# Performance work log

Measured on AMD Instinct MI355X. Metric: run time of the kernel, lower is better.

The kernel has to match this reference:

```python
import jax, jax.numpy as jnp
import numpy as np

N_NODES = 100000

def _gcn_norm(edge_index, num_nodes):
    # PyG GCNConv: add self-loops, symmetric normalization deg^-1/2 A_hat deg^-1/2
    loop = jnp.arange(num_nodes, dtype=edge_index.dtype)
    src = jnp.concatenate([edge_index[0], loop])  # [E+N]
    dst = jnp.concatenate([edge_index[1], loop])  # [E+N]
    deg = jax.ops.segment_sum(jnp.ones(dst.shape[0], jnp.float32), dst, num_segments=num_nodes)
    dis = jnp.where(deg > 0, jax.lax.rsqrt(deg), 0.0)
    norm = dis[src] * dis[dst]  # [E+N]
    return src, dst, norm

def _gcn_layer(x, W, b, src, dst, norm, num_nodes):
    xw = x @ W                                   # [N, H] dense GEMM first (out_dim <= in_dim)
    msg = xw[src] * norm[:, None]                # gather + scale per edge
    out = jax.ops.segment_sum(msg, dst, num_segments=num_nodes)  # scatter-add
    return out + b

def setup_inputs() -> dict:
    key = jax.random.key(0)
    ks = jax.random.split(key, 6)
    E = 1600000
    return {
        "x": jax.random.normal(ks[0], (N_NODES, 512), jnp.float32),
        "edge_index": jax.random.randint(ks[1], (2, E), 0, N_NODES, dtype=jnp.int64),
        "W1": jax.random.normal(ks[2], (512, 256), jnp.float32) * 0.04,
        "b1": jnp.zeros((256,), jnp.float32),
        "W2": jax.random.normal(ks[3], (256, 256), jnp.float32) * 0.06,
        "b2": jnp.zeros((256,), jnp.float32),
        "fc_w": jax.random.normal(ks[4], (256, 128), jnp.float32) * 0.06,
        "fc_b": jnp.zeros((128,), jnp.float32),
    }

def reference(x, edge_index, W1, b1, W2, b2, fc_w, fc_b):
    src, dst, norm = _gcn_norm(edge_index, N_NODES)
    h = jax.nn.relu(_gcn_layer(x, W1, b1, src, dst, norm, N_NODES))
    h = jax.nn.relu(_gcn_layer(h, W2, b2, src, dst, norm, N_NODES))
    return h @ fc_w + fc_b
```

## Files before the change

kernel.cpp:

```cpp
#include <hip/hip_runtime.h>


#define N_NODES 100000
constexpr int D_IN  = 512;
constexpr int D_H   = 256;
constexpr int D_OUT = 128;

typedef _Float16 f16x8 __attribute__((ext_vector_type(8)));
typedef _Float16 f16x4 __attribute__((ext_vector_type(4)));
typedef float f32x4 __attribute__((ext_vector_type(4)));


__global__ __launch_bounds__(256) void deg_count_k(const int* __restrict__ dst,
                                                   int* __restrict__ deg,
                                                   int* __restrict__ pe, int E) {
  int i = (blockIdx.x * 256 + threadIdx.x) * 4;
  if (i + 3 < E) {
    int4 d = *(const int4*)(dst + i);
    int4 p;
    p.x = atomicAdd(&deg[d.x], 1);
    p.y = atomicAdd(&deg[d.y], 1);
    p.z = atomicAdd(&deg[d.z], 1);
    p.w = atomicAdd(&deg[d.w], 1);
    *(int4*)(pe + i) = p;
  } else {
    for (int t = i; t < E; ++t) pe[t] = atomicAdd(&deg[dst[t]], 1);
  }
}

__global__ __launch_bounds__(256) void scan1_k(const int* __restrict__ deg,
                                               int* __restrict__ off,
                                               int* __restrict__ bsum,
                                               float* __restrict__ dis, int n) {
  __shared__ int ts[256];
  const int tid = threadIdx.x;
  const int base = blockIdx.x * 1024 + tid * 4;
  int v[4];
#pragma unroll
  for (int t = 0; t < 4; ++t) v[t] = (base + t < n) ? deg[base + t] : 0;
#pragma unroll
  for (int t = 0; t < 4; ++t)
    if (base + t < n) dis[base + t] = rsqrtf((float)v[t] + 1.0f);
  const int tot = v[0] + v[1] + v[2] + v[3];
  ts[tid] = tot;
  __syncthreads();
  for (int o = 1; o < 256; o <<= 1) {
    int t = (tid >= o) ? ts[tid - o] : 0;
    __syncthreads();
    ts[tid] += t;
    __syncthreads();
  }
  int run = ts[tid] - tot;
#pragma unroll
  for (int t = 0; t < 4; ++t) {
    if (base + t < n) off[base + t] = run;
    run += v[t];
  }
  if (tid == 255) bsum[blockIdx.x] = ts[255];
}

__global__ __launch_bounds__(128) void scan2_k(int* __restrict__ bsum, int nb) {
  __shared__ int ts[128];
  const int tid = threadIdx.x;
  const int v = (tid < nb) ? bsum[tid] : 0;
  ts[tid] = v;
  __syncthreads();
  for (int o = 1; o < 128; o <<= 1) {
    int t = (tid >= o) ? ts[tid - o] : 0;
    __syncthreads();
    ts[tid] += t;
    __syncthreads();
  }
  if (tid < nb) bsum[tid] = ts[tid] - v;
}

__global__ __launch_bounds__(256) void fill_k(const int* __restrict__ src,
                                              const int* __restrict__ dst,
                                              const int* __restrict__ pe,
                                              const int* __restrict__ off,
                                              const int* __restrict__ bsum,
                                              int* __restrict__ ssorted, int E) {
  int i = (blockIdx.x * 256 + threadIdx.x) * 4;
  if (i + 3 < E) {
    int4 s = *(const int4*)(src + i);
    int4 d = *(const int4*)(dst + i);
    int4 p = *(const int4*)(pe + i);
    ssorted[off[d.x] + bsum[d.x >> 10] + p.x] = s.x;
    ssorted[off[d.y] + bsum[d.y >> 10] + p.y] = s.y;
    ssorted[off[d.z] + bsum[d.z >> 10] + p.z] = s.z;
    ssorted[off[d.w] + bsum[d.w >> 10] + p.w] = s.w;
  } else {
    for (int t = i; t < E; ++t) {
      int d = dst[t];
      ssorted[off[d] + bsum[d >> 10] + pe[t]] = src[t];
    }
  }
}

__global__ __launch_bounds__(256) void wtrans_all_k(const float* __restrict__ W1,
                                                    const float* __restrict__ W2,
                                                    const float* __restrict__ FC,
                                                    _Float16* __restrict__ w1t,
                                                    _Float16* __restrict__ w2t,
                                                    _Float16* __restrict__ fct) {
  int i = blockIdx.x * 256 + threadIdx.x;
  if (i < 131072) {
    int k = i >> 8, n = i & 255;
    w1t[(size_t)n * 512 + k] = (_Float16)W1[i];
  } else if (i < 196608) {
    int j = i - 131072;
    int k = j >> 8, n = j & 255;
    w2t[(size_t)n * 256 + k] = (_Float16)W2[j];
  } else if (i < 229376) {
    int j = i - 196608;
    int k = j >> 7, n = j & 127;
    fct[(size_t)n * 256 + k] = (_Float16)FC[j];
  }
}

template<int BN, bool CONVERT_A, bool OUT_Y>
__global__ __launch_bounds__(512, 4) void gemm_pipe_k(
    const float* __restrict__ Af32,
    const _Float16* __restrict__ A16,
    const _Float16* __restrict__ Bt,
    const float* __restrict__ bias,
    const float* __restrict__ dis,
    float* __restrict__ C,
    _Float16* __restrict__ Y,
    int M, int K) {
  constexpr int BM = 128, BK = 32;
  constexpr int FN = BN / 64;
  constexpr int NB = BN / 128;
  constexpr int EPAD = 8;

  __shared__ __align__(16) _Float16 smem[2 * (BM + BN) * BK];
  _Float16* As = smem;
  _Float16* Bs = smem + 2 * BM * BK;
  float* epi = (float*)smem;

  const int tid  = threadIdx.x;
  const int wid  = tid >> 6, lane = tid & 63;
  const int wm   = wid >> 2, wn = wid & 3;
  const int l15  = lane & 15, l16 = lane >> 4;
  const int row0 = blockIdx.y * BM;

  f32x4 acc[4][FN];
#pragma unroll
  for (int i = 0; i < 4; ++i)
#pragma unroll
    for (int j = 0; j < FN; ++j) acc[i][j] = (f32x4){0.f, 0.f, 0.f, 0.f};

  const int arow = tid >> 2;
  const int ak8  = (tid & 3) << 3;
  const int gr   = row0 + arow;
  const int brow0 = tid >> 2;
  const int bk8   = (tid & 3) << 3;

  float4 aA0, aB0, aA1, aB1;
  f16x8  hA0, hA1;
  f16x8  b0A, b0B, b1A, b1B;

  const int nsteps = K >> 5;

#define LD_SET(kt, aA, aB, hA, bA, bB)                                         \
  {                                                                            \
    if constexpr (CONVERT_A) {                                                 \
      if (gr < M) {                                                            \
        const float* ap = Af32 + (size_t)gr * K + (kt) + ak8;                  \
        aA = *(const float4*)ap;                                               \
        aB = *(const float4*)(ap + 4);                                         \
      } else {                                                                 \
        aA = make_float4(0.f, 0.f, 0.f, 0.f);                                  \
        aB = make_float4(0.f, 0.f, 0.f, 0.f);                                  \
      }                                                                        \
    } else {                                                                   \
      if (gr < M) hA = *(const f16x8*)(A16 + (size_t)gr * K + (kt) + ak8);     \
      else        hA = (f16x8){0, 0, 0, 0, 0, 0, 0, 0};                        \
    }                                                                          \
    bA = *(const f16x8*)(Bt + (size_t)brow0 * K + (kt) + bk8);                 \
    if constexpr (NB > 1)                                                      \
      bB = *(const f16x8*)(Bt + (size_t)(brow0 + 128) * K + (kt) + bk8);       \
  }

#define WR_SET(buf, aA, aB, hA, bA, bB)                                        \
  {                                                                            \
    _Float16* as = As + (buf) * (BM * BK);                                     \
    _Float16* bs = Bs + (buf) * (BN * BK);                                     \
    if constexpr (CONVERT_A) {                                                 \
      f16x8 v;                                                                 \
      v[0] = (_Float16)aA.x; v[1] = (_Float16)aA.y;                            \
      v[2] = (_Float16)aA.z; v[3] = (_Float16)aA.w;                            \
      v[4] = (_Float16)aB.x; v[5] = (_Float16)aB.y;                            \
      v[6] = (_Float16)aB.z; v[7] = (_Float16)aB.w;                            \
      *(f16x8*)&as[arow * BK + ak8] = v;                                       \
    } else {                                                                   \
      *(f16x8*)&as[arow * BK + ak8] = hA;                                      \
    }                                                                          \
    *(f16x8*)&bs[brow0 * BK + bk8] = bA;                                       \
    if constexpr (NB > 1) *(f16x8*)&bs[(brow0 + 128) * BK + bk8] = bB;         \
  }

#define COMPUTE(buf)                                                           \
  {                                                                            \
    const _Float16* as = As + (buf) * (BM * BK);                               \
    const _Float16* bs = Bs + (buf) * (BN * BK);                               \
    f16x8 a[4], b[FN];                                                         \
    _Pragma("unroll")                                                          \
    for (int i = 0; i < 4; ++i)                                                \
      a[i] = *(const f16x8*)&as[(wm * 64 + i * 16 + l15) * BK + l16 * 8];      \
    _Pragma("unroll")                                                          \
    for (int j = 0; j < FN; ++j)                                               \
      b[j] = *(const f16x8*)&bs[(wn * (FN * 16) + j * 16 + l15) * BK + l16 * 8]; \
    _Pragma("unroll")                                                          \
    for (int i = 0; i < 4; ++i)                                                \
      _Pragma("unroll")                                                        \
      for (int j = 0; j < FN; ++j)                                             \
        acc[i][j] = __builtin_amdgcn_mfma_f32_16x16x32_f16(a[i], b[j], acc[i][j], 0, 0, 0); \
  }

  LD_SET(0, aA0, aB0, hA0, b0A, b0B);
  WR_SET(0, aA0, aB0, hA0, b0A, b0B);
  LD_SET(BK, aA1, aB1, hA1, b1A, b1B);
  __syncthreads();

  for (int tt = 0; tt < nsteps; tt += 2) {
    if (tt + 2 < nsteps) LD_SET((tt + 2) * BK, aA0, aB0, hA0, b0A, b0B);
    COMPUTE(0);
    if (tt + 1 < nsteps) WR_SET(1, aA1, aB1, hA1, b1A, b1B);
    __syncthreads();
    if (tt + 1 < nsteps) {
      if (tt + 3 < nsteps) LD_SET((tt + 3) * BK, aA1, aB1, hA1, b1A, b1B);
      COMPUTE(1);
      if (tt + 2 < nsteps) WR_SET(0, aA0, aB0, hA0, b0A, b0B);
      __syncthreads();
    }
  }
#undef LD_SET
#undef WR_SET
#undef COMPUTE

  constexpr int ESTR = BN + EPAD;
  constexpr int CPT  = BN / 16;
#pragma unroll
  for (int c = 0; c < 4; ++c) {
    if (wm == (c >> 1)) {
      const int ib = (c & 1) * 2;
#pragma unroll
      for (int ii = 0; ii < 2; ++ii) {
        const int i = ib + ii;
#pragma unroll
        for (int j = 0; j < FN; ++j) {
          const int col = wn * (FN * 16) + j * 16 + l15;
#pragma unroll
          for (int r = 0; r < 4; ++r) {
            const int lrow = ii * 16 + l16 * 4 + r;
            epi[lrow * ESTR + col] = acc[i][j][r];
          }
        }
      }
    }
    __syncthreads();
    {
      const int lrow = tid >> 4;
      const int grow = row0 + c * 32 + lrow;
      const int colb = (tid & 15) * CPT;
      if (grow < M) {
        float v[CPT];
#pragma unroll
        for (int q = 0; q < CPT; q += 4)
          *(float4*)&v[q] = *(const float4*)&epi[lrow * ESTR + colb + q];
        if constexpr (OUT_Y) {
          const float dv = dis[grow];
          f16x8 o[CPT / 8];
#pragma unroll
          for (int q = 0; q < CPT; ++q) o[q >> 3][q & 7] = (_Float16)(v[q] * dv);
#pragma unroll
          for (int q = 0; q < CPT / 8; ++q)
            *(f16x8*)(Y + (size_t)grow * BN + colb + q * 8) = o[q];
        } else {
#pragma unroll
          for (int q = 0; q < CPT; ++q) v[q] += bias[colb + q];
#pragma unroll
          for (int q = 0; q < CPT; q += 4)
            *(float4*)(C + (size_t)grow * BN + colb + q) = *(const float4*)&v[q];
        }
      }
    }
    __syncthreads();
  }
}

__global__ __launch_bounds__(256) void gather_k(const _Float16* __restrict__ y,
                                                const int* __restrict__ ssorted,
                                                const int* __restrict__ off,
                                                const int* __restrict__ bsum,
                                                const float* __restrict__ dis,
                                                const float* __restrict__ bias,
                                                _Float16* __restrict__ h,
                                                int n, int E) {
  const int gid = blockIdx.x * 256 + threadIdx.x;
  const int v = gid >> 6, lane = gid & 63;
  if (v >= n) return;

  const float dv = dis[v];
  const int fo = lane * 4;

  f16x4 sv = *(const f16x4*)(y + (size_t)v * 256 + fo);
  float4 acc = make_float4((float)sv[0], (float)sv[1], (float)sv[2], (float)sv[3]);

  const int beg = off[v] + bsum[v >> 10];
  const int end = (v + 1 < n) ? (off[v + 1] + bsum[(v + 1) >> 10]) : E;
  const int ne = end - beg;

  for (int j0 = 0; j0 < ne; j0 += 64) {
    const int rem = ne - j0;
    const int cnt = rem < 64 ? rem : 64;
    int s_l = 0;
    if (lane < cnt) s_l = ssorted[beg + j0 + lane];

    int k = 0;
    for (; k + 8 <= cnt; k += 8) {
      f16x4 yv[8];
#pragma unroll
      for (int u = 0; u < 8; ++u) {
        const int s = __shfl(s_l, k + u);
        yv[u] = *(const f16x4*)(y + (size_t)s * 256 + fo);
      }
#pragma unroll
      for (int u = 0; u < 8; ++u) {
        acc.x += (float)yv[u][0];
        acc.y += (float)yv[u][1];
        acc.z += (float)yv[u][2];
        acc.w += (float)yv[u][3];
      }
    }
    for (; k < cnt; ++k) {
      const int s = __shfl(s_l, k);
      const f16x4 yv = *(const f16x4*)(y + (size_t)s * 256 + fo);
      acc.x += (float)yv[0];
      acc.y += (float)yv[1];
      acc.z += (float)yv[2];
      acc.w += (float)yv[3];
    }
  }

  const float4 b = *(const float4*)(bias + fo);
  f16x4 o;
  o[0] = (_Float16)fmaxf(fmaf(dv, acc.x, b.x), 0.f);
  o[1] = (_Float16)fmaxf(fmaf(dv, acc.y, b.y), 0.f);
  o[2] = (_Float16)fmaxf(fmaf(dv, acc.z, b.z), 0.f);
  o[3] = (_Float16)fmaxf(fmaf(dv, acc.w, b.w), 0.f);
  *(f16x4*)(h + (size_t)v * 256 + fo) = o;
}

extern "C" void kernel_launch(void* const* d_in, const int* in_sizes, int n_in,
                              void* d_out, int out_size, void* d_ws, size_t ws_size,
                              hipStream_t stream) {
  const float* x    = (const float*)d_in[0];
  const int*   ei   = (const int*)d_in[1];
  const float* W1   = (const float*)d_in[2];
  const float* b1   = (const float*)d_in[3];
  const float* W2   = (const float*)d_in[4];
  const float* b2   = (const float*)d_in[5];
  const float* fc_w = (const float*)d_in[6];
  const float* fc_b = (const float*)d_in[7];
  float* out = (float*)d_out;

  const int E = in_sizes[1] / 2;
  const int* src = ei;
  const int* dst = ei + E;
  const int N = N_NODES;

  char* p = (char*)d_ws;
  int*   deg     = (int*)p;            p += (size_t)N * 4;
  float* dis     = (float*)p;          p += (size_t)N * 4;
  int*   off     = (int*)p;            p += (size_t)(N + 1) * 4;
  int*   pe      = (int*)p;            p += (size_t)E * 4;
  int*   ssorted = (int*)p;            p += (size_t)E * 4;
  int*   bsum    = (int*)p;            p += 512;
  p = (char*)(((size_t)p + 255) & ~(size_t)255);
  _Float16* w1t = (_Float16*)p;        p += (size_t)D_H   * D_IN * 2;
  _Float16* w2t = (_Float16*)p;        p += (size_t)D_H   * D_H  * 2;
  _Float16* fct = (_Float16*)p;        p += (size_t)D_OUT * D_H  * 2;
  p = (char*)(((size_t)p + 255) & ~(size_t)255);
  _Float16* y16 = (_Float16*)p;        p += (size_t)N * D_H * 2;
  _Float16* h16 = (_Float16*)p;        p += (size_t)N * D_H * 2;

  wtrans_all_k<<<896, 256, 0, stream>>>(W1, W2, fc_w, w1t, w2t, fct);

  const int NB1 = (N + 1023) / 1024;
  const int EB4 = ((E + 3) / 4 + 255) / 256;
  hipMemsetAsync(deg, 0, N * sizeof(int), stream);
  deg_count_k<<<EB4, 256, 0, stream>>>(dst, deg, pe, E);
  scan1_k<<<NB1, 256, 0, stream>>>(deg, off, bsum, dis, N);
  scan2_k<<<1, 128, 0, stream>>>(bsum, NB1);
  fill_k<<<EB4, 256, 0, stream>>>(src, dst, pe, off, bsum, ssorted, E);

  const int node_wave_blocks = (N * 64 + 255) / 256;
  const int MB = (N + 127) / 128;
  const dim3 gg(1, MB);

  gemm_pipe_k<256, true, true><<<gg, 512, 0, stream>>>(
      x, nullptr, w1t, nullptr, dis, nullptr, y16, N, D_IN);
  gather_k<<<node_wave_blocks, 256, 0, stream>>>(y16, ssorted, off, bsum, dis, b1, h16, N, E);

  gemm_pipe_k<256, false, true><<<gg, 512, 0, stream>>>(
      nullptr, h16, w2t, nullptr, dis, nullptr, y16, N, D_H);
  gather_k<<<node_wave_blocks, 256, 0, stream>>>(y16, ssorted, off, bsum, dis, b2, h16, N, E);

  gemm_pipe_k<128, false, false><<<gg, 512, 0, stream>>>(
      nullptr, h16, fct, fc_b, nullptr, out, nullptr, N, D_H);
}
```

Before: 519.7 us.

## Load GEMM tiles directly to LDS with swizzle and pre-convert x to fp16

Result: faster. 505.4 us (-2.7%).

```diff
diff --git a/kernel.cpp b/kernel.cpp
--- a/kernel.cpp
+++ b/kernel.cpp
@@ -5,11 +5,33 @@
 constexpr int D_IN  = 512;
 constexpr int D_H   = 256;
 constexpr int D_OUT = 128;
+constexpr int M_PAD = 100096;
 
 typedef _Float16 f16x8 __attribute__((ext_vector_type(8)));
 typedef _Float16 f16x4 __attribute__((ext_vector_type(4)));
 typedef float f32x4 __attribute__((ext_vector_type(4)));
 
+#define GLD16(SRC, DST) __builtin_amdgcn_global_load_lds(                      \
+    (const __attribute__((address_space(1))) void*)(SRC),                      \
+    (__attribute__((address_space(3))) void*)(DST), 16, 0, 0)
+
+__global__ __launch_bounds__(256) void cvt_x_k(const float* __restrict__ x,
+                                               _Float16* __restrict__ x16) {
+  size_t i = ((size_t)blockIdx.x * 256 + threadIdx.x) * 8;
+  const size_t valid = (size_t)N_NODES * D_IN;
+  if (i < valid) {
+    float4 a = *(const float4*)(x + i);
+    float4 b = *(const float4*)(x + i + 4);
+    f16x8 v;
+    v[0] = (_Float16)a.x; v[1] = (_Float16)a.y;
+    v[2] = (_Float16)a.z; v[3] = (_Float16)a.w;
+    v[4] = (_Float16)b.x; v[5] = (_Float16)b.y;
+    v[6] = (_Float16)b.z; v[7] = (_Float16)b.w;
+    *(f16x8*)(x16 + i) = v;
+  } else if (i < (size_t)M_PAD * D_IN) {
+    *(f16x8*)(x16 + i) = (f16x8){0, 0, 0, 0, 0, 0, 0, 0};
+  }
+}
 
 __global__ __launch_bounds__(256) void deg_count_k(const int* __restrict__ dst,
                                                    int* __restrict__ deg,
@@ -118,9 +140,8 @@
   }
 }
 
-template<int BN, bool CONVERT_A, bool OUT_Y>
-__global__ __launch_bounds__(512, 4) void gemm_pipe_k(
-    const float* __restrict__ Af32,
+template<int BN, bool OUT_Y>
+__global__ __launch_bounds__(512, 4) void gemm_glds_k(
     const _Float16* __restrict__ A16,
     const _Float16* __restrict__ Bt,
     const float* __restrict__ bias,
@@ -129,115 +150,75 @@
     _Float16* __restrict__ Y,
     int M, int K) {
   constexpr int BM = 128, BK = 32;
-  constexpr int FN = BN / 64;
-  constexpr int NB = BN / 128;
-  constexpr int EPAD = 8;
-
-  __shared__ __align__(16) _Float16 smem[2 * (BM + BN) * BK];
+  constexpr int FN  = BN / 64;
+  constexpr int NBI = BN / 128;
+  constexpr int ASZ = BM * BK;
+  constexpr int BSZ = BN * BK;
+  constexpr int EPAD = 4;
+
+  __shared__ __align__(16) _Float16 smem[2 * (ASZ + BSZ)];
   _Float16* As = smem;
-  _Float16* Bs = smem + 2 * BM * BK;
+  _Float16* Bs = smem + 2 * ASZ;
   float* epi = (float*)smem;
 
   const int tid  = threadIdx.x;
-  const int wid  = tid >> 6, lane = tid & 63;
-  const int wm   = wid >> 2, wn = wid & 3;
+  const int w    = tid >> 6, lane = tid & 63;
+  const int wm   = w >> 2, wn = w & 3;
   const int l15  = lane & 15, l16 = lane >> 4;
   const int row0 = blockIdx.y * BM;
 
+  const int lr = lane >> 2, lg = lane & 3;
+  const int arow  = w * 16 + lr;
+  const int brow0 = w * (NBI * 16) + lr;
+  const int brow1 = brow0 + 16;
+  const _Float16* srcA  = A16 + (size_t)(row0 + arow) * K + ((lg ^ (arow & 3)) << 3);
+  const _Float16* srcB0 = Bt + (size_t)brow0 * K + ((lg ^ (brow0 & 3)) << 3);
+  const _Float16* srcB1 = Bt + (size_t)brow1 * K + ((lg ^ (brow1 & 3)) << 3);
+  _Float16* dstA  = &As[(w * 16) * BK];
+  _Float16* dstB0 = &Bs[(w * (NBI * 16)) * BK];
+  _Float16* dstB1 = &Bs[(w * (NBI * 16) + 16) * BK];
+
   f32x4 acc[4][FN];
 #pragma unroll
   for (int i = 0; i < 4; ++i)
 #pragma unroll
     for (int j = 0; j < FN; ++j) acc[i][j] = (f32x4){0.f, 0.f, 0.f, 0.f};
 
-  const int arow = tid >> 2;
-  const int ak8  = (tid & 3) << 3;
-  const int gr   = row0 + arow;
-  const int brow0 = tid >> 2;
-  const int bk8   = (tid & 3) << 3;
-
-  float4 aA0, aB0, aA1, aB1;
-  f16x8  hA0, hA1;
-  f16x8  b0A, b0B, b1A, b1B;
-
   const int nsteps = K >> 5;
 
-#define LD_SET(kt, aA, aB, hA, bA, bB)                                         \
-  {                                                                            \
-    if constexpr (CONVERT_A) {                                                 \
-      if (gr < M) {                                                            \
-        const float* ap = Af32 + (size_t)gr * K + (kt) + ak8;                  \
-        aA = *(const float4*)ap;                                               \
-        aB = *(const float4*)(ap + 4);                                         \
-      } else {                                                                 \
-        aA = make_float4(0.f, 0.f, 0.f, 0.f);                                  \
-        aB = make_float4(0.f, 0.f, 0.f, 0.f);                                  \
-      }                                                                        \
-    } else {                                                                   \
-      if (gr < M) hA = *(const f16x8*)(A16 + (size_t)gr * K + (kt) + ak8);     \
-      else        hA = (f16x8){0, 0, 0, 0, 0, 0, 0, 0};                        \
-    }                                                                          \
-    bA = *(const f16x8*)(Bt + (size_t)brow0 * K + (kt) + bk8);                 \
-    if constexpr (NB > 1)                                                      \
-      bB = *(const f16x8*)(Bt + (size_t)(brow0 + 128) * K + (kt) + bk8);       \
-  }
-
-#define WR_SET(buf, aA, aB, hA, bA, bB)                                        \
-  {                                                                            \
-    _Float16* as = As + (buf) * (BM * BK);                                     \
-    _Float16* bs = Bs + (buf) * (BN * BK);                                     \
-    if constexpr (CONVERT_A) {                                                 \
-      f16x8 v;                                                                 \
-      v[0] = (_Float16)aA.x; v[1] = (_Float16)aA.y;                            \
-      v[2] = (_Float16)aA.z; v[3] = (_Float16)aA.w;                            \
-      v[4] = (_Float16)aB.x; v[5] = (_Float16)aB.y;                            \
-      v[6] = (_Float16)aB.z; v[7] = (_Float16)aB.w;                            \
-      *(f16x8*)&as[arow * BK + ak8] = v;                                       \
-    } else {                                                                   \
-      *(f16x8*)&as[arow * BK + ak8] = hA;                                      \
-    }                                                                          \
-    *(f16x8*)&bs[brow0 * BK + bk8] = bA;                                       \
-    if constexpr (NB > 1) *(f16x8*)&bs[(brow0 + 128) * BK + bk8] = bB;         \
-  }
-
-#define COMPUTE(buf)                                                           \
-  {                                                                            \
-    const _Float16* as = As + (buf) * (BM * BK);                               \
-    const _Float16* bs = Bs + (buf) * (BN * BK);                               \
-    f16x8 a[4], b[FN];                                                         \
-    _Pragma("unroll")                                                          \
-    for (int i = 0; i < 4; ++i)                                                \
-      a[i] = *(const f16x8*)&as[(wm * 64 + i * 16 + l15) * BK + l16 * 8];      \
-    _Pragma("unroll")                                                          \
-    for (int j = 0; j < FN; ++j)                                               \
-      b[j] = *(const f16x8*)&bs[(wn * (FN * 16) + j * 16 + l15) * BK + l16 * 8]; \
-    _Pragma("unroll")                                                          \
-    for (int i = 0; i < 4; ++i)                                                \
-      _Pragma("unroll")                                                        \
-      for (int j = 0; j < FN; ++j)                                             \
-        acc[i][j] = __builtin_amdgcn_mfma_f32_16x16x32_f16(a[i], b[j], acc[i][j], 0, 0, 0); \
-  }
-
-  LD_SET(0, aA0, aB0, hA0, b0A, b0B);
-  WR_SET(0, aA0, aB0, hA0, b0A, b0B);
-  LD_SET(BK, aA1, aB1, hA1, b1A, b1B);
+  auto stage = [&](int t) {
+    const int kt = t << 5;
+    const int pa = (t & 1) * ASZ, pb = (t & 1) * BSZ;
+    GLD16(srcA + kt, dstA + pa);
+    GLD16(srcB0 + kt, dstB0 + pb);
+    if constexpr (NBI == 2) GLD16(srcB1 + kt, dstB1 + pb);
+  };
+
+  stage(0);
   __syncthreads();
 
-  for (int tt = 0; tt < nsteps; tt += 2) {
-    if (tt + 2 < nsteps) LD_SET((tt + 2) * BK, aA0, aB0, hA0, b0A, b0B);
-    COMPUTE(0);
-    if (tt + 1 < nsteps) WR_SET(1, aA1, aB1, hA1, b1A, b1B);
-    __syncthreads();
-    if (tt + 1 < nsteps) {
-      if (tt + 3 < nsteps) LD_SET((tt + 3) * BK, aA1, aB1, hA1, b1A, b1B);
-      COMPUTE(1);
-      if (tt + 2 < nsteps) WR_SET(0, aA0, aB0, hA0, b0A, b0B);
-      __syncthreads();
-    }
-  }
-#undef LD_SET
-#undef WR_SET
-#undef COMPUTE
+  for (int t = 0; t < nsteps; ++t) {
+    if (t + 1 < nsteps) stage(t + 1);
+    const _Float16* as = As + (t & 1) * ASZ;
+    const _Float16* bs = Bs + (t & 1) * BSZ;
+    f16x8 a[4], b[FN];
+#pragma unroll
+    for (int i = 0; i < 4; ++i) {
+      const int r = wm * 64 + i * 16 + l15;
+      a[i] = *(const f16x8*)&as[r * BK + ((l16 ^ (r & 3)) << 3)];
+    }
+#pragma unroll
+    for (int j = 0; j < FN; ++j) {
+      const int n = wn * (FN * 16) + j * 16 + l15;
+      b[j] = *(const f16x8*)&bs[n * BK + ((l16 ^ (n & 3)) << 3)];
+    }
+#pragma unroll
+    for (int i = 0; i < 4; ++i)
+#pragma unroll
+      for (int j = 0; j < FN; ++j)
+        acc[i][j] = __builtin_amdgcn_mfma_f32_16x16x32_f16(a[i], b[j], acc[i][j], 0, 0, 0);
+    __syncthreads();
+  }
 
   constexpr int ESTR = BN + EPAD;
   constexpr int CPT  = BN / 16;
@@ -383,9 +364,11 @@
   _Float16* w2t = (_Float16*)p;        p += (size_t)D_H   * D_H  * 2;
   _Float16* fct = (_Float16*)p;        p += (size_t)D_OUT * D_H  * 2;
   p = (char*)(((size_t)p + 255) & ~(size_t)255);
-  _Float16* y16 = (_Float16*)p;        p += (size_t)N * D_H * 2;
-  _Float16* h16 = (_Float16*)p;        p += (size_t)N * D_H * 2;
-
+  _Float16* x16 = (_Float16*)p;        p += (size_t)M_PAD * D_IN * 2;
+  _Float16* y16 = (_Float16*)p;        p += (size_t)M_PAD * D_H * 2;
+  _Float16* h16 = (_Float16*)p;        p += (size_t)M_PAD * D_H * 2;
+
+  cvt_x_k<<<(M_PAD * (D_IN / 8) + 255) / 256, 256, 0, stream>>>(x, x16);
   wtrans_all_k<<<896, 256, 0, stream>>>(W1, W2, fc_w, w1t, w2t, fct);
 
   const int NB1 = (N + 1023) / 1024;
@@ -397,17 +380,16 @@
   fill_k<<<EB4, 256, 0, stream>>>(src, dst, pe, off, bsum, ssorted, E);
 
   const int node_wave_blocks = (N * 64 + 255) / 256;
-  const int MB = (N + 127) / 128;
-  const dim3 gg(1, MB);
-
-  gemm_pipe_k<256, true, true><<<gg, 512, 0, stream>>>(
-      x, nullptr, w1t, nullptr, dis, nullptr, y16, N, D_IN);
+  const dim3 gg(1, M_PAD / 128);
+
+  gemm_glds_k<256, true><<<gg, 512, 0, stream>>>(
+      x16, w1t, nullptr, dis, nullptr, y16, N, D_IN);
   gather_k<<<node_wave_blocks, 256, 0, stream>>>(y16, ssorted, off, bsum, dis, b1, h16, N, E);
 
-  gemm_pipe_k<256, false, true><<<gg, 512, 0, stream>>>(
-      nullptr, h16, w2t, nullptr, dis, nullptr, y16, N, D_H);
+  gemm_glds_k<256, true><<<gg, 512, 0, stream>>>(
+      h16, w2t, nullptr, dis, nullptr, y16, N, D_H);
   gather_k<<<node_wave_blocks, 256, 0, stream>>>(y16, ssorted, off, bsum, dis, b2, h16, N, E);
 
-  gemm_pipe_k<128, false, false><<<gg, 512, 0, stream>>>(
-      nullptr, h16, fct, fc_b, nullptr, out, nullptr, N, D_H);
-}
+  gemm_glds_k<128, false><<<gg, 512, 0, stream>>>(
+      h16, fct, fc_b, nullptr, out, nullptr, N, D_H);
+}
```
